# Kernel tuning notes

Hardware: AMD Instinct MI355X
Metric: run time of the kernel (lower is better)

The kernel has to match this reference:

```python
import jax, jax.numpy as jnp
import numpy as np

N_NODES = 100000
N_EDGES = 1200000
D = 64
BN_EPS = 1e-5


def setup_inputs() -> dict:
    key = jax.random.key(0)
    ks = jax.random.split(key, 6)
    x = jax.random.normal(ks[0], (N_NODES, D), dtype=jnp.float32)
    edge_index = jax.random.randint(ks[1], (2, N_EDGES), 0, N_NODES, dtype=jnp.int64)
    # Linear params (Kaiming-uniform style scale)
    lim = 1.0 / np.sqrt(D)
    W = jax.random.uniform(ks[2], (D, D), dtype=jnp.float32, minval=-lim, maxval=lim)
    b = jax.random.uniform(ks[3], (D,), dtype=jnp.float32, minval=-lim, maxval=lim)
    gamma = jnp.ones((D,), dtype=jnp.float32)
    beta = jnp.zeros((D,), dtype=jnp.float32)
    C = jax.random.normal(ks[4], (D, D), dtype=jnp.float32) * 0.1
    return {"x": x, "edge_index": edge_index, "W": W, "b": b,
            "gamma": gamma, "beta": beta, "C": C}


def reference(x, edge_index, W, b, gamma, beta, C):
    n = x.shape[0]
    src, dst = edge_index[0], edge_index[1]
    # SimpleConv(aggr='mean', combine_root='sum'): mean over incoming messages + root
    msg_sum = jax.ops.segment_sum(x[src], dst, num_segments=n)            # [N, D]
    deg = jax.ops.segment_sum(jnp.ones_like(src, dtype=x.dtype), dst, num_segments=n)
    agg = msg_sum / jnp.maximum(deg, 1.0)[:, None]
    h = x + agg
    # Linear
    h = h @ W.T + b
    # BatchNorm1d (training mode: batch stats, biased variance)
    mean = jnp.mean(h, axis=0)
    var = jnp.mean((h - mean) ** 2, axis=0)
    h = (h - mean) * jax.lax.rsqrt(var + BN_EPS) * gamma + beta
    # AsymSwiGLU gate
    gate = jax.nn.sigmoid(h @ C)
    return gate * h
```

## Files before the change

kernel.cpp:

```cpp
#include <hip/hip_runtime.h>
#include <math.h>

#define D 64
#define BN_EPS 1e-5f

#define NBITS 7
#define BINSZ 128
#define MAXBINS 800
#define CAP 2048
#define CHUNK 4096
#define BUCKET 48
#define OP 68
#define WP 72

typedef short bf16x8 __attribute__((ext_vector_type(8)));
typedef float f32x4 __attribute__((ext_vector_type(4)));

__device__ __forceinline__ unsigned f2bf(float f) {
    unsigned u = __float_as_uint(f);
    return (u + 0x7FFFu + ((u >> 16) & 1u)) >> 16;
}
__device__ __forceinline__ float bf2f(unsigned short h) {
    return __uint_as_float(((unsigned)h) << 16);
}
__device__ __forceinline__ bf16x8 cvt8f(const float* __restrict__ p) {
    float4 a = ((const float4*)p)[0];
    float4 b = ((const float4*)p)[1];
    bf16x8 r;
    r[0] = (short)f2bf(a.x); r[1] = (short)f2bf(a.y);
    r[2] = (short)f2bf(a.z); r[3] = (short)f2bf(a.w);
    r[4] = (short)f2bf(b.x); r[5] = (short)f2bf(b.y);
    r[6] = (short)f2bf(b.z); r[7] = (short)f2bf(b.w);
    return r;
}
__device__ __forceinline__ void cvtrow16(const float* __restrict__ src,
                                         unsigned short* dst) {
    float4 a = ((const float4*)src)[0], b = ((const float4*)src)[1];
    float4 c = ((const float4*)src)[2], d = ((const float4*)src)[3];
    uint4 o0, o1;
    o0.x = f2bf(a.x) | (f2bf(a.y) << 16);
    o0.y = f2bf(a.z) | (f2bf(a.w) << 16);
    o0.z = f2bf(b.x) | (f2bf(b.y) << 16);
    o0.w = f2bf(b.z) | (f2bf(b.w) << 16);
    o1.x = f2bf(c.x) | (f2bf(c.y) << 16);
    o1.y = f2bf(c.z) | (f2bf(c.w) << 16);
    o1.z = f2bf(d.x) | (f2bf(d.y) << 16);
    o1.w = f2bf(d.z) | (f2bf(d.w) << 16);
    ((uint4*)dst)[0] = o0;
    ((uint4*)dst)[1] = o1;
}

__global__ __launch_bounds__(256) void xhalf_kernel(
    const float* __restrict__ x, unsigned short* __restrict__ xh, long long n8) {
    long long t = (long long)blockIdx.x * 256 + threadIdx.x;
    if (t >= n8) return;
    const float4* rp = (const float4*)(x + t * 8);
    float4 a = rp[0], b = rp[1];
    uint4 o;
    o.x = f2bf(a.x) | (f2bf(a.y) << 16);
    o.y = f2bf(a.z) | (f2bf(a.w) << 16);
    o.z = f2bf(b.x) | (f2bf(b.y) << 16);
    o.w = f2bf(b.z) | (f2bf(b.w) << 16);
    *(uint4*)(xh + t * 8) = o;
}

__global__ __launch_bounds__(1024) void binA_kernel(
    const int* __restrict__ ei, int* __restrict__ binCursor,
    unsigned* __restrict__ binBuf, int E, int nbins) {
    __shared__ unsigned short pos[CHUNK];
    __shared__ int hist[MAXBINS];
    __shared__ int base[MAXBINS];
    int tid = threadIdx.x;
    int c0 = blockIdx.x * CHUNK;

    for (int i = tid; i < nbins; i += 1024) hist[i] = 0;
    __syncthreads();

#pragma unroll
    for (int k = 0; k < CHUNK / 1024; ++k) {
        int i = k * 1024 + tid;
        int e = c0 + i;
        if (e < E) {
            int dst = ei[E + e];
            pos[i] = (unsigned short)atomicAdd(&hist[dst >> NBITS], 1);
        }
    }
    __syncthreads();

    for (int b = tid; b < nbins; b += 1024) {
        int h = hist[b];
        base[b] = h > 0 ? atomicAdd(&binCursor[b * 16], h) : 0;
    }
    __syncthreads();

#pragma unroll
    for (int k = 0; k < CHUNK / 1024; ++k) {
        int i = k * 1024 + tid;
        int e = c0 + i;
        if (e < E) {
            int src = ei[e];
            int dst = ei[E + e];
            int b = dst >> NBITS;
            int idx = base[b] + (int)pos[i];
            if (idx < CAP)
                binBuf[(size_t)b * CAP + idx] =
                    ((unsigned)src << NBITS) | (unsigned)(dst & (BINSZ - 1));
        }
    }
}

__global__ __launch_bounds__(256) void binSort_kernel(
    const unsigned* __restrict__ binBuf, const int* __restrict__ binCursor,
    int* __restrict__ csr, int* __restrict__ cnt, int N) {
    __shared__ int hist[BINSZ];
    int bin = blockIdx.x, tid = threadIdx.x;
    int nodeBase = bin << NBITS;
    int nrows = N - nodeBase; if (nrows > BINSZ) nrows = BINSZ;
    if (tid < BINSZ) hist[tid] = 0;
    __syncthreads();
    int nE = binCursor[bin * 16]; if (nE > CAP) nE = CAP;
    const unsigned* eb = binBuf + (size_t)bin * CAP;
    for (int i = tid; i < nE; i += 256) {
        unsigned r = eb[i];
        int dl = (int)(r & (BINSZ - 1));
        int src = (int)(r >> NBITS);
        int p = atomicAdd(&hist[dl], 1);
        if (p < BUCKET) csr[(size_t)(nodeBase + dl) * BUCKET + p] = src;
    }
    __syncthreads();
    for (int r = tid; r < nrows; r += 256) cnt[nodeBase + r] = hist[r];
}

__global__ __launch_bounds__(256) void gather_kernel(
    const unsigned short* __restrict__ xh,
    const int* __restrict__ csr, const int* __restrict__ cnt,
    float* __restrict__ hpre, int N) {
    int node = blockIdx.x * 4 + (threadIdx.x >> 6);
    if (node >= N) return;
    int d = threadIdx.x & 63;
    int deg = cnt[node];
    deg = __builtin_amdgcn_readfirstlane(deg);
    int trips = deg < BUCKET ? deg : BUCKET;
    int sidx = d < BUCKET ? csr[(size_t)node * BUCKET + d] : 0;
    const unsigned short* xb = xh + d;
    float acc[8];
#pragma unroll
    for (int u = 0; u < 8; ++u) acc[u] = 0.f;
    int j = 0;
    for (; j + 7 < trips; j += 8) {
#pragma unroll
        for (int u = 0; u < 8; ++u) {
            int s = __builtin_amdgcn_readlane(sidx, j + u);
            acc[u] += bf2f(xb[(size_t)s * D]);
        }
    }
    if (j + 3 < trips) {
#pragma unroll
        for (int u = 0; u < 4; ++u) {
            int s = __builtin_amdgcn_readlane(sidx, j + u);
            acc[u] += bf2f(xb[(size_t)s * D]);
        }
        j += 4;
    }
    for (; j < trips; ++j) {
        int s = __builtin_amdgcn_readlane(sidx, j);
        acc[0] += bf2f(xb[(size_t)s * D]);
    }
    float sum = ((acc[0] + acc[1]) + (acc[2] + acc[3])) +
                ((acc[4] + acc[5]) + (acc[6] + acc[7]));
    float invd = deg > 0 ? 1.0f / (float)deg : 1.0f;
    float root = bf2f(xb[(size_t)node * D]);
    hpre[(size_t)node * D + d] = root + sum * invd;
}

__global__ __launch_bounds__(256) void linMFMA_kernel(
    float* __restrict__ h, const float* __restrict__ W,
    const float* __restrict__ bias, float* __restrict__ partial, int N) {
    __shared__ float tile[64 * OP];
    __shared__ unsigned short wt[64 * WP];
    __shared__ float psum[4 * 128];
    int tid = threadIdx.x;
    int lane = tid & 63;
    int w = tid >> 6;
    int ar = lane & 15, g = lane >> 4;
    int rbase = blockIdx.x << 6;
    int nrows = N - rbase; if (nrows > 64) nrows = 64;

#pragma unroll
    for (int it = 0; it < 4; ++it) {
        int u = it * 256 + tid;
        int r = u >> 4, c = u & 15;
        float4 v = (r < nrows)
            ? *(const float4*)(h + (size_t)(rbase + r) * D + c * 4)
            : make_float4(0.f, 0.f, 0.f, 0.f);
        *(float4*)(tile + r * OP + c * 4) = v;
    }
    {
        int r = tid >> 2, q = tid & 3;
        cvtrow16(W + (size_t)r * D + q * 16, wt + r * WP + q * 16);
    }
    __syncthreads();

    bool valid = (rbase + w * 16) < N;
    f32x4 acc[4];
    if (valid) {
        const float* arow = tile + (w * 16 + ar) * OP + 8 * g;
        bf16x8 a0 = cvt8f(arow);
        bf16x8 a1 = cvt8f(arow + 32);
#pragma unroll
        for (int t = 0; t < 4; ++t) {
            bf16x8 b0 = *(const bf16x8*)(wt + (t * 16 + ar) * WP + 8 * g);
            bf16x8 b1 = *(const bf16x8*)(wt + (t * 16 + ar) * WP + 32 + 8 * g);
            float bj = bias[t * 16 + ar];
            acc[t][0] = bj; acc[t][1] = bj; acc[t][2] = bj; acc[t][3] = bj;
            acc[t] = __builtin_amdgcn_mfma_f32_16x16x32_bf16(a0, b0, acc[t], 0, 0, 0);
            acc[t] = __builtin_amdgcn_mfma_f32_16x16x32_bf16(a1, b1, acc[t], 0, 0, 0);
        }
    }
    __syncthreads();

    if (valid) {
#pragma unroll
        for (int t = 0; t < 4; ++t) {
#pragma unroll
            for (int r = 0; r < 4; ++r)
                tile[(w * 16 + 4 * g + r) * OP + t * 16 + ar] = acc[t][r];
            float s = acc[t][0] + acc[t][1] + acc[t][2] + acc[t][3];
            float q = acc[t][0] * acc[t][0] + acc[t][1] * acc[t][1] +
                      acc[t][2] * acc[t][2] + acc[t][3] * acc[t][3];
            s += __shfl_xor(s, 16); s += __shfl_xor(s, 32);
            q += __shfl_xor(q, 16); q += __shfl_xor(q, 32);
            if (lane < 16) {
                psum[w * 128 + t * 16 + lane] = s;
                psum[w * 128 + 64 + t * 16 + lane] = q;
            }
        }
    } else {
        psum[w * 128 + lane] = 0.f;
        psum[w * 128 + 64 + lane] = 0.f;
    }
    __syncthreads();

#pragma unroll
    for (int it = 0; it < 4; ++it) {
        int u = it * 256 + tid;
        int r = u >> 4, c = u & 15;
        if (r < nrows)
            *(float4*)(h + (size_t)(rbase + r) * D + c * 4) =
                *(const float4*)(tile + r * OP + c * 4);
    }
    if (tid < 128)
        partial[(size_t)blockIdx.x * 128 + tid] =
            psum[tid] + psum[128 + tid] + psum[256 + tid] + psum[384 + tid];
}

__global__ __launch_bounds__(256) void reduceBN_kernel(
    const float* __restrict__ partial, const float* __restrict__ gamma,
    const float* __restrict__ beta, float* __restrict__ ss,
    int nWG, float inv_n) {
    __shared__ float rs[256], rq[256];
    int f = blockIdx.x;
    int tid = threadIdx.x;
    float s = 0.f, q = 0.f;
    for (int w = tid; w < nWG; w += 256) {
        s += partial[(size_t)w * 128 + f];
        q += partial[(size_t)w * 128 + 64 + f];
    }
    rs[tid] = s; rq[tid] = q;
    __syncthreads();
    for (int st = 128; st > 0; st >>= 1) {
        if (tid < st) { rs[tid] += rs[tid + st]; rq[tid] += rq[tid + st]; }
        __syncthreads();
    }
    if (tid == 0) {
        float mean = rs[0] * inv_n;
        float var = rq[0] * inv_n - mean * mean;
        float rstd = rsqrtf(var + BN_EPS);
        float sc = gamma[f] * rstd;
        ss[f] = sc;
        ss[64 + f] = beta[f] - mean * sc;
    }
}

__global__ __launch_bounds__(256) void gateMFMA_kernel(
    float* __restrict__ h, const float* __restrict__ ss,
    const float* __restrict__ C, int N) {
    __shared__ float tile[64 * OP];
    __shared__ unsigned short ct[64 * WP];
    int tid = threadIdx.x;
    int lane = tid & 63;
    int w = tid >> 6;
    int ar = lane & 15, g = lane >> 4;
    int rbase = blockIdx.x << 6;
    int nrows = N - rbase; if (nrows > 64) nrows = 64;

#pragma unroll
    for (int it = 0; it < 4; ++it) {
        int u = it * 256 + tid;
        int r = u >> 4, c = u & 15;
        float4 v = (r < nrows)
            ? *(const float4*)(h + (size_t)(rbase + r) * D + c * 4)
            : make_float4(0.f, 0.f, 0.f, 0.f);
        *(float4*)(tile + r * OP + c * 4) = v;
    }
    {
        int k = tid >> 2, q = tid & 3;
        const float* cp = C + (size_t)k * D + q * 16;
#pragma unroll
        for (int i = 0; i < 16; ++i)
            ct[(q * 16 + i) * WP + k] = (unsigned short)f2bf(cp[i]);
    }
    __syncthreads();

    bool valid = (rbase + w * 16) < N;
    f32x4 acc[4];
    if (valid) {
        const float* arow = tile + (w * 16 + ar) * OP + 8 * g;
        float4 s0 = *(const float4*)(ss + 8 * g);
        float4 s1 = *(const float4*)(ss + 8 * g + 4);
        float4 o0 = *(const float4*)(ss + 64 + 8 * g);
        float4 o1 = *(const float4*)(ss + 64 + 8 * g + 4);
        float4 v0 = ((const float4*)arow)[0];
        float4 v1 = ((const float4*)arow)[1];
        bf16x8 a0, a1;
        a0[0] = (short)f2bf(v0.x * s0.x + o0.x);
        a0[1] = (short)f2bf(v0.y * s0.y + o0.y);
        a0[2] = (short)f2bf(v0.z * s0.z + o0.z);
        a0[3] = (short)f2bf(v0.w * s0.w + o0.w);
        a0[4] = (short)f2bf(v1.x * s1.x + o1.x);
        a0[5] = (short)f2bf(v1.y * s1.y + o1.y);
        a0[6] = (short)f2bf(v1.z * s1.z + o1.z);
        a0[7] = (short)f2bf(v1.w * s1.w + o1.w);
        float4 t0 = *(const float4*)(ss + 32 + 8 * g);
        float4 t1 = *(const float4*)(ss + 32 + 8 * g + 4);
        float4 u0 = *(const float4*)(ss + 96 + 8 * g);
        float4 u1 = *(const float4*)(ss + 96 + 8 * g + 4);
        float4 w0 = ((const float4*)(arow + 32))[0];
        float4 w1 = ((const float4*)(arow + 32))[1];
        a1[0] = (short)f2bf(w0.x * t0.x + u0.x);
        a1[1] = (short)f2bf(w0.y * t0.y + u0.y);
        a1[2] = (short)f2bf(w0.z * t0.z + u0.z);
        a1[3] = (short)f2bf(w0.w * t0.w + u0.w);
        a1[4] = (short)f2bf(w1.x * t1.x + u1.x);
        a1[5] = (short)f2bf(w1.y * t1.y + u1.y);
        a1[6] = (short)f2bf(w1.z * t1.z + u1.z);
        a1[7] = (short)f2bf(w1.w * t1.w + u1.w);
#pragma unroll
        for (int t = 0; t < 4; ++t) {
            bf16x8 b0 = *(const bf16x8*)(ct + (t * 16 + ar) * WP + 8 * g);
            bf16x8 b1 = *(const bf16x8*)(ct + (t * 16 + ar) * WP + 32 + 8 * g);
            acc[t][0] = 0.f; acc[t][1] = 0.f; acc[t][2] = 0.f; acc[t][3] = 0.f;
            acc[t] = __builtin_amdgcn_mfma_f32_16x16x32_bf16(a0, b0, acc[t], 0, 0, 0);
            acc[t] = __builtin_amdgcn_mfma_f32_16x16x32_bf16(a1, b1, acc[t], 0, 0, 0);
        }
#pragma unroll
        for (int t = 0; t < 4; ++t) {
            float scC = ss[t * 16 + ar];
            float shC = ss[64 + t * 16 + ar];
#pragma unroll
            for (int r = 0; r < 4; ++r) {
                int idx = (w * 16 + 4 * g + r) * OP + t * 16 + ar;
                float hn = tile[idx] * scC + shC;
                float gg = 1.0f / (1.0f + __expf(-acc[t][r]));
                tile[idx] = gg * hn;
            }
        }
    }
    __syncthreads();

#pragma unroll
    for (int it = 0; it < 4; ++it) {
        int u = it * 256 + tid;
        int r = u >> 4, c = u & 15;
        if (r < nrows)
            *(float4*)(h + (size_t)(rbase + r) * D + c * 4) =
                *(const float4*)(tile + r * OP + c * 4);
    }
}

extern "C" void kernel_launch(void* const* d_in, const int* in_sizes, int n_in,
                              void* d_out, int out_size, void* d_ws, size_t ws_size,
                              hipStream_t stream) {
    const float* x     = (const float*)d_in[0];
    const int*   ei    = (const int*)d_in[1];
    const float* W     = (const float*)d_in[2];
    const float* b     = (const float*)d_in[3];
    const float* gamma = (const float*)d_in[4];
    const float* beta  = (const float*)d_in[5];
    const float* C     = (const float*)d_in[6];
    float* out = (float*)d_out;

    const int N = in_sizes[0] / D;
    const int E = in_sizes[1] / 2;
    const int nbins = (N + BINSZ - 1) >> NBITS;
    const int nWGlin = (N + 63) / 64;

    int*            binCursor = (int*)d_ws;
    float*          ss        = (float*)(binCursor + (size_t)nbins * 16);
    int*            cnt       = (int*)(ss + 128);
    int*            csr       = cnt + N;
    unsigned*       binBuf    = (unsigned*)(csr + (size_t)N * BUCKET);
    float*          partial   = (float*)(binBuf + (size_t)nbins * CAP);
    unsigned short* xh        = (unsigned short*)(partial + (size_t)nWGlin * 128);

    hipMemsetAsync(d_ws, 0, ((size_t)nbins * 16 + 128) * sizeof(int), stream);

    {
        long long n8 = (long long)N * D / 8;
        xhalf_kernel<<<(int)((n8 + 255) / 256), 256, 0, stream>>>(x, xh, n8);
    }
    binA_kernel<<<(E + CHUNK - 1) / CHUNK, 1024, 0, stream>>>(ei, binCursor, binBuf, E, nbins);
    binSort_kernel<<<nbins, 256, 0, stream>>>(binBuf, binCursor, csr, cnt, N);
    gather_kernel<<<(N + 3) / 4, 256, 0, stream>>>(xh, csr, cnt, out, N);
    linMFMA_kernel<<<nWGlin, 256, 0, stream>>>(out, W, b, partial, N);
    reduceBN_kernel<<<64, 256, 0, stream>>>(partial, gamma, beta, ss, nWGlin, 1.0f / (float)N);
    gateMFMA_kernel<<<(N + 63) / 64, 256, 0, stream>>>(out, ss, C, N);
}
```

Before: 121.2 us.

## Gather neighbor rows with 8-byte vector loads across four lane groups

Restructures the per-node gather so each wavefront splits into four 16-lane groups. Each lane loads four bf16 features at once with a uint2 load, and each group handles a different neighbor. Up to 12 loads per lane are issued before any accumulation to raise memory-level parallelism, and partial sums are combined with cross-group xor shuffles. This replaces one 2-byte scalar load per lane per neighbor and adds vector stores, at the cost of more registers and a shuffle reduction.

Result: faster. 116.9 us (-3.6%).

```diff
diff --git a/kernel.cpp b/kernel.cpp
--- a/kernel.cpp
+++ b/kernel.cpp
@@ -137,40 +137,55 @@
     float* __restrict__ hpre, int N) {
     int node = blockIdx.x * 4 + (threadIdx.x >> 6);
     if (node >= N) return;
-    int d = threadIdx.x & 63;
+    int l = threadIdx.x & 63;
+    int c = l & 15;
+    int g = l >> 4;
     int deg = cnt[node];
     deg = __builtin_amdgcn_readfirstlane(deg);
     int trips = deg < BUCKET ? deg : BUCKET;
-    int sidx = d < BUCKET ? csr[(size_t)node * BUCKET + d] : 0;
-    const unsigned short* xb = xh + d;
-    float acc[8];
-#pragma unroll
-    for (int u = 0; u < 8; ++u) acc[u] = 0.f;
-    int j = 0;
-    for (; j + 7 < trips; j += 8) {
-#pragma unroll
-        for (int u = 0; u < 8; ++u) {
-            int s = __builtin_amdgcn_readlane(sidx, j + u);
-            acc[u] += bf2f(xb[(size_t)s * D]);
-        }
-    }
-    if (j + 3 < trips) {
-#pragma unroll
-        for (int u = 0; u < 4; ++u) {
-            int s = __builtin_amdgcn_readlane(sidx, j + u);
-            acc[u] += bf2f(xb[(size_t)s * D]);
-        }
-        j += 4;
-    }
-    for (; j < trips; ++j) {
-        int s = __builtin_amdgcn_readlane(sidx, j);
-        acc[0] += bf2f(xb[(size_t)s * D]);
-    }
-    float sum = ((acc[0] + acc[1]) + (acc[2] + acc[3])) +
-                ((acc[4] + acc[5]) + (acc[6] + acc[7]));
+    int sidx = l < BUCKET ? csr[(size_t)node * BUCKET + l] : 0;
+    float a0 = 0.f, a1 = 0.f, a2 = 0.f, a3 = 0.f;
+    if (trips > 0) {
+        int nq = (trips + 3) >> 2;
+        int last = trips - 1;
+        uint2 v[12];
+#pragma unroll
+        for (int q = 0; q < 12; ++q) {
+            if (q < nq) {
+                int r = 4 * q + g;
+                int rc = r < trips ? r : last;
+                int s = __shfl(sidx, rc);
+                v[q] = *(const uint2*)(xh + (size_t)s * D + c * 4);
+            }
+        }
+#pragma unroll
+        for (int q = 0; q < 12; ++q) {
+            if (q < nq) {
+                int r = 4 * q + g;
+                if (r < trips) {
+                    unsigned lo = v[q].x, hi = v[q].y;
+                    a0 += __uint_as_float(lo << 16);
+                    a1 += __uint_as_float(lo & 0xFFFF0000u);
+                    a2 += __uint_as_float(hi << 16);
+                    a3 += __uint_as_float(hi & 0xFFFF0000u);
+                }
+            }
+        }
+    }
+    a0 += __shfl_xor(a0, 16); a0 += __shfl_xor(a0, 32);
+    a1 += __shfl_xor(a1, 16); a1 += __shfl_xor(a1, 32);
+    a2 += __shfl_xor(a2, 16); a2 += __shfl_xor(a2, 32);
+    a3 += __shfl_xor(a3, 16); a3 += __shfl_xor(a3, 32);
     float invd = deg > 0 ? 1.0f / (float)deg : 1.0f;
-    float root = bf2f(xb[(size_t)node * D]);
-    hpre[(size_t)node * D + d] = root + sum * invd;
+    if (g == 0) {
+        uint2 rt = *(const uint2*)(xh + (size_t)node * D + c * 4);
+        float4 o;
+        o.x = __uint_as_float(rt.x << 16)         + a0 * invd;
+        o.y = __uint_as_float(rt.x & 0xFFFF0000u) + a1 * invd;
+        o.z = __uint_as_float(rt.y << 16)         + a2 * invd;
+        o.w = __uint_as_float(rt.y & 0xFFFF0000u) + a3 * invd;
+        *(float4*)(hpre + (size_t)node * D + c * 4) = o;
+    }
 }
 
 __global__ __launch_bounds__(256) void linMFMA_kernel(
```
